# Optimization experiments

Measured on AMD Instinct MI355X. Metric: run time of the kernel, lower is better.

Reference implementation:

```python
import jax, jax.numpy as jnp
import numpy as np

B, S, D, H = 2, 2048, 1024, 16
HD = D // H  # head dim


def approx_gelu(x):
    return x * jax.nn.sigmoid(1.702 * x)


def setup_inputs() -> dict:
    key = jax.random.key(0)
    ks = jax.random.split(key, 12)
    q = jax.random.normal(ks[0], (B, S, D), jnp.float32)
    k = jax.random.normal(ks[1], (B, S, D), jnp.float32)
    v = jax.random.normal(ks[2], (B, S, D), jnp.float32)
    mask = jnp.zeros((B, 1, S, S), jnp.float32)
    sc = 0.02
    Wq = jax.random.normal(ks[3], (H, D, HD), jnp.float32) * sc
    bq = jax.random.normal(ks[4], (H, HD), jnp.float32) * sc
    Wk = jax.random.normal(ks[5], (H, D, HD), jnp.float32) * sc
    bk = jax.random.normal(ks[6], (H, HD), jnp.float32) * sc
    Wv = jax.random.normal(ks[7], (H, D, HD), jnp.float32) * sc
    bv = jax.random.normal(ks[8], (H, HD), jnp.float32) * sc
    Wo = jax.random.normal(ks[9], (D, D), jnp.float32) * sc
    bo = jax.random.normal(ks[10], (D,), jnp.float32) * sc
    return {"q": q, "k": k, "v": v, "mask": mask, "Wq": Wq, "bq": bq,
            "Wk": Wk, "bk": bk, "Wv": Wv, "bv": bv, "Wo": Wo, "bo": bo}


def reference(q, k, v, mask, Wq, bq, Wk, bk, Wv, bv, Wo, bo):
    # Per-head Q/K/V dense (no activation on projections, matching source).
    qh = jnp.einsum('bsd,hde->bhse', q, Wq) + bq[None, :, None, :]  # [B,H,S,HD]
    kh = jnp.einsum('bsd,hde->bhse', k, Wk) + bk[None, :, None, :]
    vh = jnp.einsum('bsd,hde->bhse', v, Wv) + bv[None, :, None, :]
    scale = 1.0 / jnp.sqrt(jnp.asarray(HD, qh.dtype))
    logits = jnp.einsum('bhse,bhte->bhst', qh, kh) * scale + mask  # [B,H,S,S]
    attn = jax.nn.softmax(logits, axis=-1)
    heads = jnp.einsum('bhst,bhte->bhse', attn, vh)  # [B,H,S,HD]
    # concat heads -> [B,S,D]
    x = jnp.transpose(heads, (0, 2, 1, 3)).reshape(q.shape[0], q.shape[1], D)
    return approx_gelu(x @ Wo + bo)
```

## Files before the change

kernel.cpp:

```cpp
#include <hip/hip_runtime.h>
#include <stdint.h>


typedef __bf16 bf16x8 __attribute__((ext_vector_type(8)));
typedef __bf16 bf16x4 __attribute__((ext_vector_type(4)));
typedef float f32x4 __attribute__((ext_vector_type(4)));
typedef float f32x16 __attribute__((ext_vector_type(16)));
typedef unsigned u32x4 __attribute__((ext_vector_type(4)));

static constexpr float L2E  = 1.4426950408889634f;
static constexpr float QSCL = 0.18033688011112042f;
static constexpr float GELC = -2.4554669595930157f;

__device__ __forceinline__ void async_load16(const void* g, void* l) {
    __builtin_amdgcn_global_load_lds(
        (const __attribute__((address_space(1))) unsigned int*)(uintptr_t)g,
        (__attribute__((address_space(3))) unsigned int*)(unsigned int)(uintptr_t)l,
        16, 0, 0);
}

template <int ROWS>
__device__ __forceinline__ void stage_tile(const __bf16* g, int ld, __bf16* lds, int tid) {
#pragma unroll
    for (int r = 0; r < ROWS / 32; ++r) {
        int p = r * 4096 + tid * 16;
        int row = p >> 7;
        int kbp = p & 127;
        int kbl = kbp ^ ((row & 7) << 4);
        async_load16((const char*)(g + (size_t)row * ld) + kbl,
                     (char*)lds + (p & ~1023));
    }
}

__device__ __forceinline__ bf16x8 lds_frag(const __bf16* base, int row, int kb) {
    return *(const bf16x8*)((const char*)base + (row << 7) + (kb ^ ((row & 7) << 4)));
}

__device__ __forceinline__ unsigned cvtpk(float a, float b) {
    unsigned d;
    asm("v_cvt_pk_bf16_f32 %0, %1, %2" : "=v"(d) : "v"(a), "v"(b));
    return d;
}
__device__ __forceinline__ void pswap(unsigned& a, unsigned& b) {
    asm("v_permlane32_swap_b32 %0, %1" : "+v"(a), "+v"(b));
}

__device__ __forceinline__ void stage_a_f32(const float* g, __bf16* lds, int tid) {
    int rsub = tid >> 3;
    int c8 = (tid & 7) * 8;
#pragma unroll
    for (int pass = 0; pass < 4; ++pass) {
        int row = pass * 32 + rsub;
        const float* src = g + (size_t)row * 1024 + c8;
        f32x4 a = *(const f32x4*)src;
        f32x4 b = *(const f32x4*)(src + 4);
        u32x4 pk;
        pk[0] = cvtpk(a[0], a[1]);
        pk[1] = cvtpk(a[2], a[3]);
        pk[2] = cvtpk(b[0], b[1]);
        pk[3] = cvtpk(b[2], b[3]);
        *(u32x4*)((char*)lds + row * 128 + ((c8 * 2) ^ ((row & 7) << 4))) = pk;
    }
}


__global__ __launch_bounds__(256) void mask_flags(const float* __restrict__ m,
                                                  unsigned* __restrict__ flags) {
    int i = blockIdx.x * 256 + threadIdx.x;
    f32x4 v = ((const f32x4*)m)[i];
    bool nz = (v[0] != 0.f) | (v[1] != 0.f) | (v[2] != 0.f) | (v[3] != 0.f);
    if (nz) {
        size_t i4 = (size_t)i * 4;
        int b = (int)(i4 >> 22);
        int rem = (int)(i4 & 4194303);
        int qq = rem >> 11, kv = rem & 2047;
        atomicOr(flags + (b * 16 + (qq >> 7)) * 32 + (kv >> 6), 1u);
    }
}

__global__ __launch_bounds__(256) void pack_w4(const float* __restrict__ Wq,
                                               const float* __restrict__ Wk,
                                               const float* __restrict__ Wv,
                                               const float* __restrict__ Wo,
                                               __bf16* __restrict__ w3,
                                               __bf16* __restrict__ wo) {
    __shared__ __bf16 T[64][72];
    int tid = threadIdx.x;
    int z = blockIdx.z;
    int k0 = blockIdx.x * 64;
    if (z < 3) {
        int h = blockIdx.y;
        const float* W = z == 0 ? Wq : (z == 1 ? Wk : Wv);
#pragma unroll
        for (int it = 0; it < 4; ++it) {
            int idx = it * 1024 + tid * 4;
            int r = idx >> 6, e = idx & 63;
            f32x4 val = *(const f32x4*)(W + ((size_t)h * 1024 + k0 + r) * 64 + e);
#pragma unroll
            for (int j = 0; j < 4; ++j) T[r][e + j] = (__bf16)val[j];
        }
        __syncthreads();
        int e2 = tid >> 2, kc = (tid & 3) * 16;
        bf16x8 o0, o1;
#pragma unroll
        for (int i = 0; i < 8; ++i) { o0[i] = T[kc + i][e2]; o1[i] = T[kc + 8 + i][e2]; }
        __bf16* dst = w3 + ((size_t)z << 20) + (size_t)(h * 64 + e2) * 1024 + k0 + kc;
        *(bf16x8*)dst = o0;
        *(bf16x8*)(dst + 8) = o1;
    } else {
        int n0 = blockIdx.y * 64;
#pragma unroll
        for (int it = 0; it < 4; ++it) {
            int idx = it * 1024 + tid * 4;
            int r = idx >> 6, e = idx & 63;
            f32x4 val = *(const f32x4*)(Wo + (size_t)(k0 + r) * 1024 + n0 + e);
#pragma unroll
            for (int j = 0; j < 4; ++j) T[r][e + j] = (__bf16)val[j];
        }
        __syncthreads();
        int e2 = tid >> 2, kc = (tid & 3) * 16;
        bf16x8 o0, o1;
#pragma unroll
        for (int i = 0; i < 8; ++i) { o0[i] = T[kc + i][e2]; o1[i] = T[kc + 8 + i][e2]; }
        __bf16* dst = wo + (size_t)(n0 + e2) * 1024 + k0 + kc;
        *(bf16x8*)dst = o0;
        *(bf16x8*)(dst + 8) = o1;
    }
}

__global__ __launch_bounds__(256) void gemm_qkv(
    const float* __restrict__ qf32, const float* __restrict__ kf32,
    const float* __restrict__ vf32, const __bf16* __restrict__ w3,
    const float* __restrict__ bq, const float* __restrict__ bk,
    const float* __restrict__ bv,
    __bf16* __restrict__ Qp, __bf16* __restrict__ Kp, __bf16* __restrict__ Vp) {
    __shared__ __bf16 As[128 * 64];
    __shared__ __bf16 Bs[128 * 64];
    int z = blockIdx.z;
    const float* A = z == 0 ? qf32 : (z == 1 ? kf32 : vf32);
    const __bf16* Bt = w3 + ((size_t)z << 20);
    const float* bias = z == 0 ? bq : (z == 1 ? bk : bv);
    float sc = z == 0 ? QSCL : 1.0f;

    int tid = threadIdx.x;
    int w = tid >> 6, lane = tid & 63, lg = lane >> 4, lr = lane & 15;
    int wr = (w >> 1) * 64, wc = (w & 1) * 64;
    int m0 = blockIdx.x * 128, n0 = blockIdx.y * 128;
    f32x4 acc[4][4] = {};
    for (int k0 = 0; k0 < 1024; k0 += 64) {
        __syncthreads();
        stage_a_f32(A + (size_t)m0 * 1024 + k0, As, tid);
        stage_tile<128>(Bt + (size_t)n0 * 1024 + k0, 1024, Bs, tid);
        __syncthreads();
#pragma unroll
        for (int kk = 0; kk < 2; ++kk) {
            bf16x8 af[4], bfr[4];
#pragma unroll
            for (int t = 0; t < 4; ++t) {
                af[t] = lds_frag(As, wr + t * 16 + lr, lg * 16 + kk * 64);
                bfr[t] = lds_frag(Bs, wc + t * 16 + lr, lg * 16 + kk * 64);
            }
#pragma unroll
            for (int i = 0; i < 4; ++i)
#pragma unroll
                for (int j = 0; j < 4; ++j)
                    acc[i][j] = __builtin_amdgcn_mfma_f32_16x16x32_bf16(
                        af[i], bfr[j], acc[i][j], 0, 0, 0);
        }
    }
#pragma unroll
    for (int i = 0; i < 4; ++i) {
        int mb = m0 + wr + i * 16 + lg * 4;
        int b = mb >> 11, s = mb & 2047;
#pragma unroll
        for (int j = 0; j < 4; ++j) {
            int n = n0 + wc + j * 16 + lr;
            float bvv = bias[n];
            int h = n >> 6, e = n & 63;
            int bh = b * 16 + h;
            if (z == 2) {
                size_t addr = ((size_t)bh * 32 + (s >> 6)) * 4096 + (e >> 5) * 2048 +
                              ((s >> 4) & 3) * 512 + ((s >> 3) & 1) * 256 +
                              (e & 31) * 8 + (s & 7);
                bf16x4 o;
#pragma unroll
                for (int r = 0; r < 4; ++r) o[r] = (__bf16)(acc[i][j][r] + bvv);
                *(bf16x4*)(Vp + addr) = o;
            } else {
                __bf16* out = z == 0 ? Qp : Kp;
                size_t base = ((size_t)bh * 64 + (s >> 5)) * 2048 + (e >> 4) * 512 +
                              ((e >> 3) & 1) * 256 + (s & 31) * 8 + (e & 7);
#pragma unroll
                for (int r = 0; r < 4; ++r)
                    out[base + r * 8] = (__bf16)((acc[i][j][r] + bvv) * sc);
            }
        }
    }
}

__global__ __launch_bounds__(256) void gemm_out(const __bf16* __restrict__ A,
                                                const __bf16* __restrict__ Bt,
                                                const float* __restrict__ bias,
                                                float* __restrict__ dst) {
    __shared__ __bf16 As[64 * 64];
    __shared__ __bf16 Bs[128 * 64];
    int tid = threadIdx.x;
    int w = tid >> 6, lane = tid & 63, lg = lane >> 4, lr = lane & 15;
    int wr = (w >> 1) * 32, wc = (w & 1) * 64;
    int m0 = blockIdx.x * 64, n0 = blockIdx.y * 128;
    f32x4 acc[2][4] = {};
    for (int k0 = 0; k0 < 1024; k0 += 64) {
        __syncthreads();
        stage_tile<64>(A + (size_t)m0 * 1024 + k0, 1024, As, tid);
        stage_tile<128>(Bt + (size_t)n0 * 1024 + k0, 1024, Bs, tid);
        __syncthreads();
#pragma unroll
        for (int kk = 0; kk < 2; ++kk) {
            bf16x8 af[2], bfr[4];
#pragma unroll
            for (int t = 0; t < 2; ++t)
                af[t] = lds_frag(As, wr + t * 16 + lr, lg * 16 + kk * 64);
#pragma unroll
            for (int t = 0; t < 4; ++t)
                bfr[t] = lds_frag(Bs, wc + t * 16 + lr, lg * 16 + kk * 64);
#pragma unroll
            for (int i = 0; i < 2; ++i)
#pragma unroll
                for (int j = 0; j < 4; ++j)
                    acc[i][j] = __builtin_amdgcn_mfma_f32_16x16x32_bf16(
                        af[i], bfr[j], acc[i][j], 0, 0, 0);
        }
    }
#pragma unroll
    for (int i = 0; i < 2; ++i) {
        int mb = m0 + wr + i * 16 + lg * 4;
#pragma unroll
        for (int j = 0; j < 4; ++j) {
            int n = n0 + wc + j * 16 + lr;
            float bvv = bias[n];
#pragma unroll
            for (int r = 0; r < 4; ++r) {
                float v = acc[i][j][r] + bvv;
                float g = v / (1.f + exp2f(GELC * v));
                dst[(size_t)(mb + r) * 1024 + n] = g;
            }
        }
    }
}

__global__ __launch_bounds__(256) void attn_kernel(
    const __bf16* __restrict__ Qp, const __bf16* __restrict__ Kp,
    const __bf16* __restrict__ Vp, const float* __restrict__ mask,
    const unsigned* __restrict__ flags,
    __bf16* __restrict__ Op0, __bf16* __restrict__ Op1,
    float* __restrict__ lacc) {
    int tid = threadIdx.x;
    int w = tid >> 6, l = tid & 63;
    int q31 = l & 31, hi = l >> 5;
    int i = blockIdx.x;
    int xcd = i & 7, j = i >> 3;
    int group = (j >> 4) * 8 + xcd;
    int qt = j & 15;
    int bh = group & 31, z = group >> 5;
    int b = bh >> 4, h = bh & 15;
    int qw = qt * 128 + w * 32;

    const __bf16* Qb = Qp + ((size_t)bh * 64 + (qw >> 5)) * 2048 + l * 8;
    bf16x8 qf[4];
#pragma unroll
    for (int kk = 0; kk < 4; ++kk) qf[kk] = *(const bf16x8*)(Qb + kk * 512);

    const __bf16* Kb = Kp + ((size_t)bh * 64 + z * 32) * 2048 + l * 8;
    const __bf16* Vb = Vp + ((size_t)bh * 32 + z * 16) * 4096 + l * 8;
    const float* mrow = mask + (size_t)b * 4194304 + (size_t)(qw + q31) * 2048 + (z << 10) + hi * 4;
    const unsigned* flg = flags + (b * 16 + qt) * 32 + z * 16;

    f32x16 O[2] = {};
    float la0 = 0.f, la1 = 0.f;

    bf16x8 kf[2][4];
#pragma unroll
    for (int mt = 0; mt < 2; ++mt)
#pragma unroll
        for (int kk = 0; kk < 4; ++kk)
            kf[mt][kk] = *(const bf16x8*)(Kb + (mt * 4 + kk) * 512);

    for (int kt = 0; kt < 16; ++kt) {
        f32x16 T[2] = {};
        __builtin_amdgcn_s_setprio(1);
#pragma unroll
        for (int kk = 0; kk < 4; ++kk)
#pragma unroll
            for (int mt = 0; mt < 2; ++mt)
                T[mt] = __builtin_amdgcn_mfma_f32_32x32x16_bf16(kf[mt][kk], qf[kk], T[mt], 0, 0, 0);
        __builtin_amdgcn_s_setprio(0);

        bf16x8 vf[2][4];
#pragma unroll
        for (int mt = 0; mt < 2; ++mt)
#pragma unroll
            for (int kk = 0; kk < 4; ++kk)
                vf[mt][kk] = *(const bf16x8*)(Vb + (size_t)kt * 4096 + (mt * 4 + kk) * 512);
        if (kt < 15) {
#pragma unroll
            for (int mt = 0; mt < 2; ++mt)
#pragma unroll
                for (int kk = 0; kk < 4; ++kk)
                    kf[mt][kk] = *(const bf16x8*)(Kb + ((size_t)(kt + 1) * 2 + mt) * 2048 + kk * 512);
        }

        unsigned fl = __builtin_amdgcn_readfirstlane(flg[kt]);
        if (fl) {
#pragma unroll
            for (int mt = 0; mt < 2; ++mt)
#pragma unroll
                for (int g = 0; g < 4; ++g) {
                    f32x4 mk = *(const f32x4*)(mrow + kt * 64 + mt * 32 + g * 8);
#pragma unroll
                    for (int c = 0; c < 4; ++c)
                        T[mt][4 * g + c] = fmaf(mk[c], L2E, T[mt][4 * g + c]);
                }
        }
#pragma unroll
        for (int g = 0; g < 4; ++g) {
            float a0 = exp2f(T[0][4 * g + 0]);
            float a1 = exp2f(T[0][4 * g + 1]);
            float a2 = exp2f(T[0][4 * g + 2]);
            float a3 = exp2f(T[0][4 * g + 3]);
            float b0 = exp2f(T[1][4 * g + 0]);
            float b1 = exp2f(T[1][4 * g + 1]);
            float b2 = exp2f(T[1][4 * g + 2]);
            float b3 = exp2f(T[1][4 * g + 3]);
            la0 += (a0 + a1) + (a2 + a3);
            la1 += (b0 + b1) + (b2 + b3);
            T[0][4 * g + 0] = a0; T[0][4 * g + 1] = a1;
            T[0][4 * g + 2] = a2; T[0][4 * g + 3] = a3;
            T[1][4 * g + 0] = b0; T[1][4 * g + 1] = b1;
            T[1][4 * g + 2] = b2; T[1][4 * g + 3] = b3;
        }

        bf16x8 pf[4];
#pragma unroll
        for (int kk = 0; kk < 4; ++kk) {
            int mt = kk >> 1;
            int gA = (2 * kk) & 3, gB = gA + 1;
            unsigned x0 = cvtpk(T[mt][4 * gA + 0], T[mt][4 * gA + 1]);
            unsigned x1 = cvtpk(T[mt][4 * gA + 2], T[mt][4 * gA + 3]);
            unsigned y0 = cvtpk(T[mt][4 * gB + 0], T[mt][4 * gB + 1]);
            unsigned y1 = cvtpk(T[mt][4 * gB + 2], T[mt][4 * gB + 3]);
            pswap(x0, y0);
            pswap(x1, y1);
            u32x4 packed; packed[0] = x0; packed[1] = x1; packed[2] = y0; packed[3] = y1;
            pf[kk] = __builtin_bit_cast(bf16x8, packed);
        }

        __builtin_amdgcn_s_setprio(1);
#pragma unroll
        for (int kk = 0; kk < 4; ++kk)
#pragma unroll
            for (int mt = 0; mt < 2; ++mt)
                O[mt] = __builtin_amdgcn_mfma_f32_32x32x16_bf16(vf[mt][kk], pf[kk], O[mt], 0, 0, 0);
        __builtin_amdgcn_s_setprio(0);
    }

    float l_acc = la0 + la1;
    l_acc += __shfl_xor(l_acc, 32, 64);
    if (hi == 0)
        lacc[((size_t)z * 32 + b * 16 + h) * 2048 + qw + q31] = l_acc;
    __bf16* Ob = (z ? Op1 : Op0) + (((size_t)(b * 16 + h)) * 2048 + qw + q31) * 64 + hi * 4;
#pragma unroll
    for (int mt = 0; mt < 2; ++mt)
#pragma unroll
        for (int g = 0; g < 4; ++g) {
            bf16x4 o;
#pragma unroll
            for (int c = 0; c < 4; ++c) o[c] = (__bf16)O[mt][4 * g + c];
            *(bf16x4*)(Ob + mt * 32 + g * 8) = o;
        }
}

__global__ __launch_bounds__(256) void attn_norm(const __bf16* __restrict__ Op0,
                                                 const __bf16* __restrict__ Op1,
                                                 const float* __restrict__ lacc,
                                                 __bf16* __restrict__ x) {
    int idx = blockIdx.x * 256 + threadIdx.x;
    int b = idx >> 19;
    int rem = idx & 524287;
    int h = rem >> 15;
    int s = (rem >> 4) & 2047;
    int e0 = (rem & 15) * 4;
    size_t base = (((size_t)(b * 16 + h)) * 2048 + s) * 64 + e0;
    bf16x4 a = *(const bf16x4*)(Op0 + base);
    bf16x4 c = *(const bf16x4*)(Op1 + base);
    size_t li = ((size_t)(b * 16 + h)) * 2048 + s;
    float inv = 1.0f / (lacc[li] + lacc[65536 + li]);
    bf16x4 r;
#pragma unroll
    for (int j = 0; j < 4; ++j)
        r[j] = (__bf16)(((float)a[j] + (float)c[j]) * inv);
    *(bf16x4*)(x + ((size_t)b * 2048 + s) * 1024 + h * 64 + e0) = r;
}


extern "C" void kernel_launch(void* const* d_in, const int* in_sizes, int n_in,
                              void* d_out, int out_size, void* d_ws, size_t ws_size,
                              hipStream_t stream) {
    const float* q    = (const float*)d_in[0];
    const float* k    = (const float*)d_in[1];
    const float* v    = (const float*)d_in[2];
    const float* mask = (const float*)d_in[3];
    const float* Wq   = (const float*)d_in[4];
    const float* bq   = (const float*)d_in[5];
    const float* Wk   = (const float*)d_in[6];
    const float* bk   = (const float*)d_in[7];
    const float* Wv   = (const float*)d_in[8];
    const float* bv   = (const float*)d_in[9];
    const float* Wo   = (const float*)d_in[10];
    const float* bo   = (const float*)d_in[11];

    char* ws = (char*)d_ws;
    __bf16* Op0 = (__bf16*)(ws + (0ull  << 20));
    __bf16* Op1 = (__bf16*)(ws + (8ull  << 20));
    __bf16* xp  = (__bf16*)(ws + (16ull << 20));
    __bf16* w3  = (__bf16*)(ws + (24ull << 20));
    __bf16* wo  = (__bf16*)(ws + (30ull << 20));
    __bf16* Qpk = (__bf16*)(ws + (32ull << 20));
    __bf16* Kpk = (__bf16*)(ws + (40ull << 20));
    __bf16* Vpk = (__bf16*)(ws + (48ull << 20));
    float*  laccp = (float*)(ws + (56ull << 20));
    unsigned* flagp = (unsigned*)(ws + (56ull << 20) + (512ull << 10));

    pack_w4<<<dim3(16, 16, 4), 256, 0, stream>>>(Wq, Wk, Wv, Wo, w3, wo);
    hipMemsetAsync(flagp, 0, 4096, stream);
    mask_flags<<<8192, 256, 0, stream>>>(mask, flagp);

    gemm_qkv<<<dim3(32, 8, 3), 256, 0, stream>>>(q, k, v, w3, bq, bk, bv,
                                                 Qpk, Kpk, Vpk);

    attn_kernel<<<dim3(1024), 256, 0, stream>>>(Qpk, Kpk, Vpk, mask, flagp,
                                                Op0, Op1, laccp);
    attn_norm<<<4096, 256, 0, stream>>>(Op0, Op1, laccp, xp);

    gemm_out<<<dim3(64, 8), 256, 0, stream>>>(xp, wo, bo, (float*)d_out);
}
```

Baseline: 161.4 us.

## Stage fp32 A tiles via async LDS loads and use raw v_exp_f32

After: 146.0 us. 9.6% less time.

```diff
diff --git a/kernel.cpp b/kernel.cpp
--- a/kernel.cpp
+++ b/kernel.cpp
@@ -11,6 +11,14 @@
 static constexpr float L2E  = 1.4426950408889634f;
 static constexpr float QSCL = 0.18033688011112042f;
 static constexpr float GELC = -2.4554669595930157f;
+
+#if __has_builtin(__builtin_amdgcn_exp2f)
+__device__ __forceinline__ float fexp2(float x) { return __builtin_amdgcn_exp2f(x); }
+#else
+__device__ __forceinline__ float fexp2(float x) {
+    float r; asm("v_exp_f32 %0, %1" : "=v"(r) : "v"(x)); return r;
+}
+#endif
 
 __device__ __forceinline__ void async_load16(const void* g, void* l) {
     __builtin_amdgcn_global_load_lds(
@@ -32,6 +40,18 @@
     }
 }
 
+__device__ __forceinline__ void stage_a32(const float* g, float* lds, int tid) {
+#pragma unroll
+    for (int r = 0; r < 8; ++r) {
+        int p = r * 4096 + tid * 16;
+        int row = p >> 8;
+        int cb  = p & 255;
+        int cbs = cb ^ ((row & 7) << 5);
+        async_load16((const char*)(g + (size_t)row * 1024) + cbs,
+                     (char*)lds + (p & ~1023));
+    }
+}
+
 __device__ __forceinline__ bf16x8 lds_frag(const __bf16* base, int row, int kb) {
     return *(const bf16x8*)((const char*)base + (row << 7) + (kb ^ ((row & 7) << 4)));
 }
@@ -45,22 +65,15 @@
     asm("v_permlane32_swap_b32 %0, %1" : "+v"(a), "+v"(b));
 }
 
-__device__ __forceinline__ void stage_a_f32(const float* g, __bf16* lds, int tid) {
-    int rsub = tid >> 3;
-    int c8 = (tid & 7) * 8;
-#pragma unroll
-    for (int pass = 0; pass < 4; ++pass) {
-        int row = pass * 32 + rsub;
-        const float* src = g + (size_t)row * 1024 + c8;
-        f32x4 a = *(const f32x4*)src;
-        f32x4 b = *(const f32x4*)(src + 4);
-        u32x4 pk;
-        pk[0] = cvtpk(a[0], a[1]);
-        pk[1] = cvtpk(a[2], a[3]);
-        pk[2] = cvtpk(b[0], b[1]);
-        pk[3] = cvtpk(b[2], b[3]);
-        *(u32x4*)((char*)lds + row * 128 + ((c8 * 2) ^ ((row & 7) << 4))) = pk;
-    }
+__device__ __forceinline__ bf16x8 frag_f32(const float* base, int row, int eo) {
+    int cb = (eo * 4) ^ ((row & 7) << 5);
+    const char* p = (const char*)base + row * 256 + cb;
+    f32x4 a = *(const f32x4*)p;
+    f32x4 b = *(const f32x4*)(p + 16);
+    u32x4 pk;
+    pk[0] = cvtpk(a[0], a[1]); pk[1] = cvtpk(a[2], a[3]);
+    pk[2] = cvtpk(b[0], b[1]); pk[3] = cvtpk(b[2], b[3]);
+    return __builtin_bit_cast(bf16x8, pk);
 }
 
 
@@ -129,15 +142,15 @@
 }
 
 __global__ __launch_bounds__(256) void gemm_qkv(
-    const float* __restrict__ qf32, const float* __restrict__ kf32,
-    const float* __restrict__ vf32, const __bf16* __restrict__ w3,
+    const float* __restrict__ qf, const float* __restrict__ kf2,
+    const float* __restrict__ vf2, const __bf16* __restrict__ w3,
     const float* __restrict__ bq, const float* __restrict__ bk,
     const float* __restrict__ bv,
     __bf16* __restrict__ Qp, __bf16* __restrict__ Kp, __bf16* __restrict__ Vp) {
-    __shared__ __bf16 As[128 * 64];
+    __shared__ float  Asf[128 * 64];
     __shared__ __bf16 Bs[128 * 64];
     int z = blockIdx.z;
-    const float* A = z == 0 ? qf32 : (z == 1 ? kf32 : vf32);
+    const float* A = z == 0 ? qf : (z == 1 ? kf2 : vf2);
     const __bf16* Bt = w3 + ((size_t)z << 20);
     const float* bias = z == 0 ? bq : (z == 1 ? bk : bv);
     float sc = z == 0 ? QSCL : 1.0f;
@@ -149,7 +162,7 @@
     f32x4 acc[4][4] = {};
     for (int k0 = 0; k0 < 1024; k0 += 64) {
         __syncthreads();
-        stage_a_f32(A + (size_t)m0 * 1024 + k0, As, tid);
+        stage_a32(A + (size_t)m0 * 1024 + k0, Asf, tid);
         stage_tile<128>(Bt + (size_t)n0 * 1024 + k0, 1024, Bs, tid);
         __syncthreads();
 #pragma unroll
@@ -157,7 +170,7 @@
             bf16x8 af[4], bfr[4];
 #pragma unroll
             for (int t = 0; t < 4; ++t) {
-                af[t] = lds_frag(As, wr + t * 16 + lr, lg * 16 + kk * 64);
+                af[t] = frag_f32(Asf, wr + t * 16 + lr, lg * 8 + kk * 32);
                 bfr[t] = lds_frag(Bs, wc + t * 16 + lr, lg * 16 + kk * 64);
             }
 #pragma unroll
@@ -241,7 +254,7 @@
 #pragma unroll
             for (int r = 0; r < 4; ++r) {
                 float v = acc[i][j][r] + bvv;
-                float g = v / (1.f + exp2f(GELC * v));
+                float g = v / (1.f + fexp2(GELC * v));
                 dst[(size_t)(mb + r) * 1024 + n] = g;
             }
         }
@@ -323,14 +336,14 @@
         }
 #pragma unroll
         for (int g = 0; g < 4; ++g) {
-            float a0 = exp2f(T[0][4 * g + 0]);
-            float a1 = exp2f(T[0][4 * g + 1]);
-            float a2 = exp2f(T[0][4 * g + 2]);
-            float a3 = exp2f(T[0][4 * g + 3]);
-            float b0 = exp2f(T[1][4 * g + 0]);
-            float b1 = exp2f(T[1][4 * g + 1]);
-            float b2 = exp2f(T[1][4 * g + 2]);
-            float b3 = exp2f(T[1][4 * g + 3]);
+            float a0 = fexp2(T[0][4 * g + 0]);
+            float a1 = fexp2(T[0][4 * g + 1]);
+            float a2 = fexp2(T[0][4 * g + 2]);
+            float a3 = fexp2(T[0][4 * g + 3]);
+            float b0 = fexp2(T[1][4 * g + 0]);
+            float b1 = fexp2(T[1][4 * g + 1]);
+            float b2 = fexp2(T[1][4 * g + 2]);
+            float b3 = fexp2(T[1][4 * g + 3]);
             la0 += (a0 + a1) + (a2 + a3);
             la1 += (b0 + b1) + (b2 + b3);
             T[0][4 * g + 0] = a0; T[0][4 * g + 1] = a1;
```
